# Kernel optimization log

Hardware: AMD Instinct MI355X
Metric: run time of the kernel (lower is better)

The kernel has to match this reference:

```python
import jax, jax.numpy as jnp
import numpy as np

BS, N, M, D = 8, 2048, 64, 1024
N_WAY, N_SHOT = 64, 5


def setup_inputs() -> dict:
    key = jax.random.key(0)
    k1, k2, k3, k4, k5 = jax.random.split(key, 5)
    return {
        "prototypes": jax.random.normal(k1, (BS, M, D), dtype=jnp.float32),
        "masktypes": jax.random.uniform(k2, (BS, M, D), dtype=jnp.float32),
        "query": jax.random.normal(k3, (BS, N, D), dtype=jnp.float32),
        "support": jax.random.normal(k4, (BS, N_WAY * N_SHOT, D), dtype=jnp.float32),
        "support_labels": jax.random.randint(k5, (BS, N_WAY * N_SHOT), 0, N_WAY, dtype=jnp.int64),
        "scale": jnp.ones((1,), dtype=jnp.float32),
        "n_way": N_WAY,
        "n_shot": N_SHOT,
    }


def reference(prototypes, masktypes, query, support, support_labels, scale, n_way, n_shot):
    # Masked squared Euclidean distance:
    #   logits[b,n,m] = sum_d (mask[b,m,d] * (query[b,n,d] - proto[b,m,d]))^2
    # Expanded via the GEMM trick to avoid the (bs,n,m,d) intermediate:
    #   = sum_d mask^2 q^2 - 2 sum_d q (mask^2 p) + sum_d (mask p)^2
    dims = prototypes.shape[-1]
    mask2 = masktypes * masktypes                       # [b,m,d]
    q_term = jnp.einsum('bnd,bmd->bnm', query * query, mask2)
    cross = jnp.einsum('bnd,bmd->bnm', query, mask2 * prototypes)
    mp = masktypes * prototypes                         # [b,m,d]
    p_term = jnp.sum(mp * mp, axis=-1)[:, None, :]      # [b,1,m]
    logits = (q_term - 2.0 * cross + p_term) / dims     # normalize=True
    return scale * logits
```

## Files before the change

### kernel.cpp

```cpp
#include <hip/hip_runtime.h>

#define BSZ 8
#define NQ 2048
#define MP 64
#define DD 1024
#define K2ALL 2048
#define BN 16
#define BK 64
#define K2 128
#define LDK 136
#define KT 16
#define NTILES (NQ / BN)

typedef __bf16 bf16x8 __attribute__((ext_vector_type(8)));
typedef float f32x4 __attribute__((ext_vector_type(4)));
typedef unsigned short us8 __attribute__((ext_vector_type(8)));

__device__ __forceinline__ unsigned short f2bf(float f) {
    union { float f; unsigned int u; } v; v.f = f;
    unsigned int u = v.u;
    return (unsigned short)((u + 0x7FFFu + ((u >> 16) & 1u)) >> 16);
}

__global__ __launch_bounds__(256) void pack_kernel(
    const float* __restrict__ proto,
    const float* __restrict__ mask,
    unsigned short* __restrict__ Pp,
    float* __restrict__ Pterm)
{
    const int row = blockIdx.x;
    const int t = threadIdx.x;

    const float4 mk = *(const float4*)(mask  + (size_t)row * DD + 4 * t);
    const float4 pr = *(const float4*)(proto + (size_t)row * DD + 4 * t);

    const float m2x = mk.x * mk.x, m2y = mk.y * mk.y,
                m2z = mk.z * mk.z, m2w = mk.w * mk.w;
    const float ax = mk.x * pr.x, ay = mk.y * pr.y,
                az = mk.z * pr.z, aw = mk.w * pr.w;
    float pacc = ax * ax + ay * ay + az * az + aw * aw;

    us8 o;
    o[0] = f2bf(m2x); o[1] = f2bf(-2.f * m2x * pr.x);
    o[2] = f2bf(m2y); o[3] = f2bf(-2.f * m2y * pr.y);
    o[4] = f2bf(m2z); o[5] = f2bf(-2.f * m2z * pr.z);
    o[6] = f2bf(m2w); o[7] = f2bf(-2.f * m2w * pr.w);
    *(us8*)(Pp + (size_t)row * K2ALL + 8 * t) = o;

    __shared__ float red[4];
    #pragma unroll
    for (int off = 32; off > 0; off >>= 1)
        pacc += __shfl_down(pacc, off, 64);
    const int lane = t & 63, w = t >> 6;
    if (lane == 0) red[w] = pacc;
    __syncthreads();
    if (t == 0) Pterm[row] = red[0] + red[1] + red[2] + red[3];
}

__global__ __launch_bounds__(256, 4) void proto_main_kernel(
    const float* __restrict__ query,
    const unsigned short* __restrict__ Pp,
    const float* __restrict__ Pterm,
    const float* __restrict__ scale,
    float* __restrict__ out)
{
    __shared__ unsigned short Qs[2][BN][LDK];

    const int tid = threadIdx.x;
    const int bid = blockIdx.x;
    const int b  = bid & 7;
    const int n0 = (bid >> 3) * BN;

    const int qrow = tid >> 4;
    const int qc   = tid & 15;
    const float* qptr = query + ((size_t)b * NQ + n0 + qrow) * DD + 4 * qc;

    const int lane = tid & 63;
    const int wid  = tid >> 6;
    const int lrow = lane & 15;
    const int lq   = (lane >> 4) * 8;

    const int mcol = 16 * wid + lrow;
    const unsigned short* bptr = Pp + ((size_t)(b * MP + mcol)) * K2ALL + lq;

    f32x4 acc = (f32x4){0.f, 0.f, 0.f, 0.f};
    float4 q[2];
    bf16x8 bv[2][4];

    const float pt = Pterm[b * MP + mcol];
    const float sc = scale[0] * (1.0f / (float)DD);

    q[0] = *(const float4*)(qptr);
    q[1] = *(const float4*)(qptr + BK);
    #pragma unroll
    for (int i = 0; i < 4; ++i)
        bv[0][i] = *(const bf16x8*)(bptr + 32 * i);

    #pragma unroll
    for (int kt = 0; kt < KT; ++kt) {
        const int cur = kt & 1;

        {
            const float4 qq = q[cur];
            us8 o;
            o[0] = f2bf(qq.x * qq.x); o[1] = f2bf(qq.x);
            o[2] = f2bf(qq.y * qq.y); o[3] = f2bf(qq.y);
            o[4] = f2bf(qq.z * qq.z); o[5] = f2bf(qq.z);
            o[6] = f2bf(qq.w * qq.w); o[7] = f2bf(qq.w);
            *(us8*)(&Qs[cur][qrow][8 * qc]) = o;
        }
        __syncthreads();

        if (kt + 2 < KT)
            q[cur] = *(const float4*)(qptr + (kt + 2) * BK);
        if (kt + 1 < KT) {
            #pragma unroll
            for (int i = 0; i < 4; ++i)
                bv[(kt + 1) & 1][i] =
                    *(const bf16x8*)(bptr + (kt + 1) * K2 + 32 * i);
        }

        #pragma unroll
        for (int i = 0; i < 4; ++i) {
            const bf16x8 a = *(const bf16x8*)(&Qs[cur][lrow][32 * i + lq]);
            acc = __builtin_amdgcn_mfma_f32_16x16x32_bf16(a, bv[cur][i], acc, 0, 0, 0);
        }
    }

    const size_t ob = ((size_t)b * NQ + (size_t)(n0 + (lane >> 4) * 4)) * MP + mcol;
    #pragma unroll
    for (int r = 0; r < 4; ++r)
        out[ob + (size_t)r * MP] = (acc[r] + pt) * sc;
}

extern "C" void kernel_launch(void* const* d_in, const int* in_sizes, int n_in,
                              void* d_out, int out_size, void* d_ws, size_t ws_size,
                              hipStream_t stream) {
    (void)in_sizes; (void)n_in; (void)ws_size; (void)out_size;
    const float* proto = (const float*)d_in[0];
    const float* mask  = (const float*)d_in[1];
    const float* query = (const float*)d_in[2];
    const float* scale = (const float*)d_in[5];
    float* out = (float*)d_out;

    unsigned short* Pp = (unsigned short*)d_ws;
    float* Pterm = (float*)((char*)d_ws + (size_t)BSZ * MP * K2ALL * 2);

    pack_kernel<<<dim3(BSZ * MP), dim3(256), 0, stream>>>(proto, mask, Pp, Pterm);
    proto_main_kernel<<<dim3(BSZ * NTILES), dim3(256), 0, stream>>>(
        query, Pp, Pterm, scale, out);
}
```

Baseline: 140.5 us.

## Stage full query tile in LDS upfront and stream B fragments with deeper prefetch

The main kernel now loads the block's entire 16-row query slice (all 16 chunks) into registers at once, converts it to bf16 pairs, and writes it to a single large LDS buffer behind one barrier. The per-k-step double-buffered LDS and its 16 syncthreads are gone. The B (packed prototype) fragments are then streamed with an 8-deep register prefetch ring feeding back-to-back MFMAs. This removes per-iteration barriers and exposes more memory parallelism, at the cost of many more registers and about 64KB of LDS per block, and the launch_bounds occupancy hint is dropped, so fewer blocks can be resident per CU.

```diff
diff --git a/kernel.cpp b/kernel.cpp
--- a/kernel.cpp
+++ b/kernel.cpp
@@ -6,10 +6,8 @@
 #define DD 1024
 #define K2ALL 2048
 #define BN 16
-#define BK 64
-#define K2 128
-#define LDK 136
-#define KT 16
+#define LDKQ 2056
+#define NSTEP 64
 #define NTILES (NQ / BN)
 
 typedef __bf16 bf16x8 __attribute__((ext_vector_type(8)));
@@ -57,14 +55,14 @@
     if (t == 0) Pterm[row] = red[0] + red[1] + red[2] + red[3];
 }
 
-__global__ __launch_bounds__(256, 4) void proto_main_kernel(
+__global__ __launch_bounds__(256) void proto_main_kernel(
     const float* __restrict__ query,
     const unsigned short* __restrict__ Pp,
     const float* __restrict__ Pterm,
     const float* __restrict__ scale,
     float* __restrict__ out)
 {
-    __shared__ unsigned short Qs[2][BN][LDK];
+    __shared__ unsigned short Qs[BN][LDKQ];
 
     const int tid = threadIdx.x;
     const int bid = blockIdx.x;
@@ -83,47 +81,41 @@
     const int mcol = 16 * wid + lrow;
     const unsigned short* bptr = Pp + ((size_t)(b * MP + mcol)) * K2ALL + lq;
 
-    f32x4 acc = (f32x4){0.f, 0.f, 0.f, 0.f};
-    float4 q[2];
-    bf16x8 bv[2][4];
+    float4 qv[16];
+    #pragma unroll
+    for (int p = 0; p < 16; ++p)
+        qv[p] = *(const float4*)(qptr + 64 * p);
 
     const float pt = Pterm[b * MP + mcol];
     const float sc = scale[0] * (1.0f / (float)DD);
 
-    q[0] = *(const float4*)(qptr);
-    q[1] = *(const float4*)(qptr + BK);
     #pragma unroll
-    for (int i = 0; i < 4; ++i)
-        bv[0][i] = *(const bf16x8*)(bptr + 32 * i);
+    for (int p = 0; p < 16; ++p) {
+        const float4 q = qv[p];
+        us8 o;
+        o[0] = f2bf(q.x * q.x); o[1] = f2bf(q.x);
+        o[2] = f2bf(q.y * q.y); o[3] = f2bf(q.y);
+        o[4] = f2bf(q.z * q.z); o[5] = f2bf(q.z);
+        o[6] = f2bf(q.w * q.w); o[7] = f2bf(q.w);
+        *(us8*)(&Qs[qrow][8 * qc + 128 * p]) = o;
+    }
+    __syncthreads();
+
+    f32x4 acc = (f32x4){0.f, 0.f, 0.f, 0.f};
+    bf16x8 bq[8];
+    #pragma unroll
+    for (int i = 0; i < 8; ++i)
+        bq[i] = *(const bf16x8*)(bptr + 32 * i);
 
     #pragma unroll
-    for (int kt = 0; kt < KT; ++kt) {
-        const int cur = kt & 1;
-
-        {
-            const float4 qq = q[cur];
-            us8 o;
-            o[0] = f2bf(qq.x * qq.x); o[1] = f2bf(qq.x);
-            o[2] = f2bf(qq.y * qq.y); o[3] = f2bf(qq.y);
-            o[4] = f2bf(qq.z * qq.z); o[5] = f2bf(qq.z);
-            o[6] = f2bf(qq.w * qq.w); o[7] = f2bf(qq.w);
-            *(us8*)(&Qs[cur][qrow][8 * qc]) = o;
-        }
-        __syncthreads();
-
-        if (kt + 2 < KT)
-            q[cur] = *(const float4*)(qptr + (kt + 2) * BK);
-        if (kt + 1 < KT) {
-            #pragma unroll
-            for (int i = 0; i < 4; ++i)
-                bv[(kt + 1) & 1][i] =
-                    *(const bf16x8*)(bptr + (kt + 1) * K2 + 32 * i);
-        }
-
+    for (int g = 0; g < NSTEP; g += 8) {
         #pragma unroll
-        for (int i = 0; i < 4; ++i) {
-            const bf16x8 a = *(const bf16x8*)(&Qs[cur][lrow][32 * i + lq]);
-            acc = __builtin_amdgcn_mfma_f32_16x16x32_bf16(a, bv[cur][i], acc, 0, 0, 0);
+        for (int j = 0; j < 8; ++j) {
+            const bf16x8 bb = bq[j];
+            if (g + 8 + j < NSTEP)
+                bq[j] = *(const bf16x8*)(bptr + 32 * (g + 8 + j));
+            const bf16x8 a = *(const bf16x8*)(&Qs[lrow][32 * (g + j) + lq]);
+            acc = __builtin_amdgcn_mfma_f32_16x16x32_bf16(a, bb, acc, 0, 0, 0);
         }
     }
 
```

New measurement: 140.6 us. About the same (+0.1%).
